# Kernel tuning notes

Measured on AMD Instinct MI355X. Metric: run time of the kernel, lower is better.

The kernel has to match this reference:

```python
import jax, jax.numpy as jnp
import numpy as np

B, C, H, W = 16, 256, 32, 32  # C == emb_dim
NUM_EMB = 8192


def setup_inputs() -> dict:
    key = jax.random.key(0)
    k1, k2 = jax.random.split(key)
    z_e = jax.random.normal(k1, (B, C, H, W), dtype=jnp.float32)
    # torch init: uniform(-1/num_emb, 1/num_emb); randn spec scaled to similar magnitude
    embedding = jax.random.uniform(k2, (NUM_EMB, C), dtype=jnp.float32,
                                   minval=-1.0 / NUM_EMB, maxval=1.0 / NUM_EMB)
    return {"z_e": z_e, "embedding": embedding}


def reference(z_e, embedding):
    num_emb, emb_dim = embedding.shape
    # [B, C, H, W] -> [B, H, W, C]
    z = jnp.transpose(z_e, (0, 2, 3, 1))
    flat = z.reshape(-1, emb_dim)  # [N, C]
    # squared L2 distances via ||z||^2 + ||e||^2 - 2 z.e  (the addmm)
    emb_sqr = jnp.sum(embedding * embedding, axis=1)            # [K]
    z_sqr = jnp.sum(flat * flat, axis=1, keepdims=True)         # [N, 1]
    distances = z_sqr + emb_sqr[None, :] - 2.0 * (flat @ embedding.T)  # [N, K]
    indices = jnp.argmin(distances, axis=1)                     # [N]
    z_q = embedding[indices].reshape(z.shape)                   # gather -> [B,H,W,C]
    z_one_hot = jax.nn.one_hot(indices, num_emb, dtype=jnp.float32)  # [N, K]
    # straight-through estimator
    z_q = z + jax.lax.stop_gradient(z_q - z)
    return (z, z_q, indices, z_one_hot)
```

## Files before the change

kernel.cpp:

```cpp
#include <hip/hip_runtime.h>
#include <stdint.h>

typedef unsigned long long u64;
typedef unsigned u32;
typedef __attribute__((ext_vector_type(8))) _Float16 half8;
typedef __attribute__((ext_vector_type(4))) float f32x4;

#define NROWS 16384
#define CDIM  256
#define NEMB  8192

#define Z_OFF   0ull
#define ZQ_OFF  4194304ull
#define IDX_OFF 8388608ull
#define OH_OFF  8404992ull

#define ES_OFF_BYTES     0
#define ZS_OFF_BYTES     32768
#define ORIENT_OFF_BYTES 98304
#define KEYSA_OFF_BYTES  131072
#define KEYSB_OFF_BYTES  4325376
#define EHL_ROW0 16128

#define ESCALE 512.0f
#define INV2SCALE 0.00390625f

#define THR_ULP 4u
#define TRIP_ULP 8u

__device__ __forceinline__ u32 fmap(float x) {
    u32 u = __float_as_uint(x);
    return (u & 0x80000000u) ? ~u : (u | 0x80000000u);
}
__device__ __forceinline__ u32 udiff(u32 a, u32 b) { return a > b ? a - b : b - a; }

__device__ __forceinline__ void gload_lds16(const char* g, char* l) {
    __builtin_amdgcn_global_load_lds(
        (const __attribute__((address_space(1))) void*)(g),
        (__attribute__((address_space(3))) void*)(l), 16, 0, 0);
}

__global__ __launch_bounds__(256) void k_transpose(const float* __restrict__ ze,
                                                   float* __restrict__ z) {
    __shared__ float T[64][65];
    int b = blockIdx.z, ct = blockIdx.x, ht = blockIdx.y;
    int c0 = ct * 64, hw0 = ht * 64;
    int lane = threadIdx.x & 63, grp = threadIdx.x >> 6;
    #pragma unroll
    for (int i = 0; i < 16; ++i) {
        int cl = grp + i * 4;
        T[cl][lane] = ze[((size_t)(b * 256 + c0 + cl)) * 1024 + hw0 + lane];
    }
    __syncthreads();
    #pragma unroll
    for (int i = 0; i < 16; ++i) {
        int hwl = grp + i * 4;
        z[((size_t)(b * 1024 + hw0 + hwl)) * 256 + c0 + lane] = T[lane][hwl];
    }
}

__device__ __forceinline__ float pw128sq(const float* __restrict__ x) {
    float r[8];
    #pragma unroll
    for (int j = 0; j < 8; ++j) r[j] = __fmul_rn(x[j], x[j]);
    #pragma unroll
    for (int i = 8; i < 128; i += 8) {
        #pragma unroll
        for (int j = 0; j < 8; ++j)
            r[j] = __fadd_rn(r[j], __fmul_rn(x[i + j], x[i + j]));
    }
    return __fadd_rn(__fadd_rn(__fadd_rn(r[0], r[1]), __fadd_rn(r[2], r[3])),
                     __fadd_rn(__fadd_rn(r[4], r[5]), __fadd_rn(r[6], r[7])));
}

__global__ __launch_bounds__(256) void k_rowsq(const float* __restrict__ X,
                                               float* __restrict__ out,
                                               int nrows) {
    int r = blockIdx.x * 256 + threadIdx.x;
    if (r >= nrows) return;
    const float* x = &X[(size_t)r * 256];
    out[r] = __fadd_rn(pw128sq(x), pw128sq(x + 128));
}

__global__ __launch_bounds__(256) void k_zsq(const float* __restrict__ ze,
                                             float* __restrict__ zs) {
    int t = blockIdx.x * 256 + threadIdx.x;
    int b = t >> 10, hw = t & 1023;
    const float* base = ze + ((size_t)b * 256) * 1024 + hw;
    float half[2];
    #pragma unroll
    for (int hB = 0; hB < 2; ++hB) {
        const float* p = base + (size_t)(hB * 128) * 1024;
        float r[8];
        #pragma unroll
        for (int j = 0; j < 8; ++j) {
            float v = p[(size_t)j * 1024];
            r[j] = __fmul_rn(v, v);
        }
        #pragma unroll
        for (int i = 8; i < 128; i += 8) {
            #pragma unroll
            for (int j = 0; j < 8; ++j) {
                float v = p[(size_t)(i + j) * 1024];
                r[j] = __fadd_rn(r[j], __fmul_rn(v, v));
            }
        }
        half[hB] = __fadd_rn(__fadd_rn(__fadd_rn(r[0], r[1]), __fadd_rn(r[2], r[3])),
                             __fadd_rn(__fadd_rn(r[4], r[5]), __fadd_rn(r[6], r[7])));
    }
    zs[t] = __fadd_rn(half[0], half[1]);
}

__global__ __launch_bounds__(256) void k_split16(const float* __restrict__ X,
                                                 char* __restrict__ H,
                                                 int nrows, float scale) {
    int t = blockIdx.x * 256 + threadIdx.x;
    if (t >= nrows * 32) return;
    int row = t >> 5, c8 = t & 31;
    const float* src = X + (size_t)row * 256 + c8 * 8;
    float4 f0 = *(const float4*)src;
    float4 f1 = *(const float4*)(src + 4);
    float f[8] = {f0.x, f0.y, f0.z, f0.w, f1.x, f1.y, f1.z, f1.w};
    union { _Float16 h[8]; uint4 v; } u;
    #pragma unroll
    for (int j = 0; j < 8; ++j)
        u.h[j] = (_Float16)(f[j] * scale);
    int rb = row >> 7, rloc = row & 127, kc = c8 >> 2, p = c8 & 3;
    size_t base = ((size_t)(rb * 8 + kc)) * 8192 + (size_t)p * 2048 + (size_t)rloc * 16;
    *(uint4*)(H + base) = u.v;
}

__global__ __launch_bounds__(256) void k_dist(const char* __restrict__ ZH,
                                              const char* __restrict__ EH,
                                              const float* __restrict__ es,
                                              const float* __restrict__ zs,
                                              u32* __restrict__ keysA,
                                              u32* __restrict__ keysB) {
    __shared__ __align__(16) char smem[21504];
    int bx = blockIdx.x;
    int by = blockIdx.y;
    int tid = threadIdx.x;
    int w = tid >> 6, lane = tid & 63;
    int p = lane >> 4, l15 = lane & 15;
    int rowhalf = (w & 1) * 64, colhalf = (w >> 1) * 64;
    int row0 = by * 128, col0 = bx * 128;

    f32x4 acc[4][4] = {};

    const char* asrc = ZH + ((size_t)(by * 8)) * 8192;
    const char* bsrc = EH + ((size_t)(bx * 8)) * 8192;

    for (int kc = 0; kc < 8; ++kc) {
        if (kc) __syncthreads();
        const char* ak = asrc + (size_t)kc * 8192;
        const char* bk = bsrc + (size_t)kc * 8192;
        #pragma unroll
        for (int it = 0; it < 2; ++it) {
            int off = it * 4096 + tid * 16;
            gload_lds16(ak + off, smem + off);
        }
        #pragma unroll
        for (int it = 0; it < 2; ++it) {
            int off = it * 4096 + tid * 16;
            gload_lds16(bk + off, smem + 8192 + off);
        }
        __syncthreads();

        half8 A[4], B[4];
        #pragma unroll
        for (int rt = 0; rt < 4; ++rt) {
            int r = rowhalf + rt * 16 + l15;
            A[rt] = *(const half8*)(smem + p * 2048 + r * 16);
        }
        #pragma unroll
        for (int ct = 0; ct < 4; ++ct) {
            int c = colhalf + ct * 16 + l15;
            B[ct] = *(const half8*)(smem + 8192 + p * 2048 + c * 16);
        }
        #pragma unroll
        for (int rt = 0; rt < 4; ++rt)
            #pragma unroll
            for (int ct = 0; ct < 4; ++ct)
                acc[rt][ct] = __builtin_amdgcn_mfma_f32_16x16x32_f16(
                    A[rt], B[ct], acc[rt][ct], 0, 0, 0);
    }
    __syncthreads();

    u32* redA = (u32*)smem;
    u32* redB = (u32*)(smem + 16896);

    float esA[4], zsB4[4], esB[4][4], zsA[4][4];
    #pragma unroll
    for (int ct = 0; ct < 4; ++ct) {
        esA[ct] = es[col0 + colhalf + ct * 16 + l15];
        #pragma unroll
        for (int reg = 0; reg < 4; ++reg)
            esB[ct][reg] = es[col0 + colhalf + ct * 16 + p * 4 + reg];
    }
    #pragma unroll
    for (int rt = 0; rt < 4; ++rt) {
        zsB4[rt] = zs[row0 + rowhalf + rt * 16 + l15];
        #pragma unroll
        for (int reg = 0; reg < 4; ++reg)
            zsA[rt][reg] = zs[row0 + rowhalf + rt * 16 + p * 4 + reg];
    }

    #pragma unroll
    for (int rt = 0; rt < 4; ++rt) {
        u32 bB = 0xffffffffu;
        #pragma unroll
        for (int reg = 0; reg < 4; ++reg) {
            u32 bA = 0xffffffffu;
            #pragma unroll
            for (int ct = 0; ct < 4; ++ct) {
                float a2 = __fmul_rn(acc[rt][ct][reg], INV2SCALE);
                float vA = __fsub_rn(__fadd_rn(zsA[rt][reg], esA[ct]), a2);
                float vB = __fsub_rn(__fadd_rn(zsB4[rt], esB[ct][reg]), a2);
                u32 fA = fmap(vA), fB = fmap(vB);
                if (fA < bA) bA = fA;
                if (fB < bB) bB = fB;
            }
            redA[(rowhalf + rt * 16 + p * 4 + reg) * 33 + (w >> 1) * 16 + l15] = bA;
        }
        redB[(rowhalf + rt * 16 + l15) * 9 + (w >> 1) * 4 + p] = bB;
    }
    __syncthreads();
    if (tid < 128) {
        u32 bA = 0xffffffffu, bB = 0xffffffffu;
        #pragma unroll
        for (int s = 0; s < 32; ++s) { u32 v = redA[tid * 33 + s]; if (v < bA) bA = v; }
        #pragma unroll
        for (int s = 0; s < 8; ++s)  { u32 v = redB[tid * 9 + s];  if (v < bB) bB = v; }
        keysA[((size_t)(row0 + tid)) * 64 + bx] = bA;
        keysB[((size_t)(row0 + tid)) * 64 + bx] = bB;
    }
}

__device__ __forceinline__ u64 exact_key4(const float* zrow, const float* __restrict__ E,
                                          const float* __restrict__ es, float zsn, int k) {
    const float4* e4 = (const float4*)&E[(size_t)k * 256];
    float dot = 0.0f;
    #pragma unroll 4
    for (int c4 = 0; c4 < 64; ++c4) {
        float4 ev = e4[c4];
        dot = fmaf(zrow[c4 * 4 + 0], ev.x, dot);
        dot = fmaf(zrow[c4 * 4 + 1], ev.y, dot);
        dot = fmaf(zrow[c4 * 4 + 2], ev.z, dot);
        dot = fmaf(zrow[c4 * 4 + 3], ev.w, dot);
    }
    float t1 = __fadd_rn(zsn, es[k]);
    float d  = __fsub_rn(t1, __fmul_rn(2.0f, dot));
    return ((u64)fmap(d) << 32) | (u32)k;
}

__global__ __launch_bounds__(256) void k_orient(const float* __restrict__ Z,
                                                const float* __restrict__ E,
                                                const float* __restrict__ es,
                                                const float* __restrict__ zs,
                                                const u32* __restrict__ keysA,
                                                const u32* __restrict__ keysB,
                                                int* __restrict__ orient) {
    __shared__ float zrow[256];
    __shared__ u32 mex[256];
    int tid = threadIdx.x;
    zrow[tid] = Z[tid];
    __syncthreads();
    int chunk = tid >> 4, sub = tid & 15;
    float zsn = zs[0];
    u32 best = 0xffffffffu;
    #pragma unroll 2
    for (int j = 0; j < 8; ++j) {
        u64 key = exact_key4(zrow, E, es, zsn, chunk * 128 + sub * 8 + j);
        u32 f = (u32)(key >> 32);
        if (f < best) best = f;
    }
    mex[tid] = best;
    __syncthreads();
    if (tid == 0) {
        int cA = 0, cB = 0;
        for (int s = 0; s < 16; ++s) {
            u32 m = 0xffffffffu;
            for (int t = 0; t < 16; ++t) { u32 v = mex[s * 16 + t]; if (v < m) m = v; }
            if (udiff(keysA[s], m) <= 2u) ++cA;
            if (udiff(keysB[s], m) <= 2u) ++cB;
        }
        *orient = (cA >= 12) ? 0 : (cB >= 12) ? 1 : 2;
    }
}

__global__ __launch_bounds__(256) void k_final(const float* __restrict__ Z,
                                               const float* __restrict__ E,
                                               const float* __restrict__ es,
                                               const float* __restrict__ zs,
                                               const u32* __restrict__ keysA,
                                               const u32* __restrict__ keysB,
                                               const int* __restrict__ orient,
                                               float* __restrict__ zq,
                                               float* __restrict__ idxf,
                                               float* __restrict__ oh) {
    __shared__ float zrow[256];
    __shared__ u32 kch[64];
    __shared__ u64 rmin[256];
    __shared__ int flaglist[64];
    __shared__ int nflag;
    __shared__ u32 mval;
    __shared__ int strip;

    int n = blockIdx.x, tid = threadIdx.x;
    int ori = *orient;
    const u32* keys = (ori == 1) ? keysB : keysA;

    zrow[tid] = Z[(size_t)n * 256 + tid];
    if (tid < 64) kch[tid] = keys[(size_t)n * 64 + tid];
    __syncthreads();
    if (tid == 0) {
        if (ori == 2) {
            nflag = 64;
            for (int s = 0; s < 64; ++s) flaglist[s] = s;
            mval = 0;
        } else {
            u32 m = 0xffffffffu;
            for (int s = 0; s < 64; ++s) if (kch[s] < m) m = kch[s];
            u32 thr = m + THR_ULP;
            int nf = 0;
            for (int s = 0; s < 64; ++s) if (kch[s] <= thr) flaglist[nf++] = s;
            nflag = nf; mval = m;
        }
    }
    __syncthreads();

    float zsn = zs[n];
    u64 best = ~0ull;
    {
        int tot = nflag * 128;
        for (int i = tid; i < tot; i += 256) {
            u64 key = exact_key4(zrow, E, es, zsn,
                                 flaglist[i >> 7] * 128 + (i & 127));
            if (key < best) best = key;
        }
    }
    rmin[tid] = best;
    __syncthreads();
    for (int s = 128; s > 0; s >>= 1) {
        if (tid < s) { if (rmin[tid + s] < rmin[tid]) rmin[tid] = rmin[tid + s]; }
        __syncthreads();
    }
    u64 ph1 = rmin[0];
    if (tid == 0)
        strip = (ori != 2) && (udiff((u32)(ph1 >> 32), mval) > TRIP_ULP);
    __syncthreads();

    if (strip) {
        best = ~0ull;
        for (int i = tid; i < NEMB; i += 256) {
            u64 key = exact_key4(zrow, E, es, zsn, i);
            if (key < best) best = key;
        }
        rmin[tid] = best;
        __syncthreads();
        for (int s = 128; s > 0; s >>= 1) {
            if (tid < s) { if (rmin[tid + s] < rmin[tid]) rmin[tid] = rmin[tid + s]; }
            __syncthreads();
        }
    }
    int idx = (int)(rmin[0] & 0xffffffffu);

    if (n >= EHL_ROW0) {
        float* ohrow = oh + (size_t)n * NEMB;
        float4 z4 = make_float4(0.f, 0.f, 0.f, 0.f);
        #pragma unroll
        for (int it = 0; it < 8; ++it)
            *(float4*)&ohrow[(it * 256 + tid) * 4] = z4;
        __syncthreads();
    }

    if (tid < 64)
        *(float4*)&zq[(size_t)n * 256 + tid * 4] =
            *(const float4*)&E[(size_t)idx * 256 + tid * 4];
    if (tid == 0) {
        idxf[n] = (float)idx;
        oh[(size_t)n * NEMB + idx] = 1.0f;
    }
}

extern "C" void kernel_launch(void* const* d_in, const int* in_sizes, int n_in,
                              void* d_out, int out_size, void* d_ws, size_t ws_size,
                              hipStream_t stream) {
    const float* ze  = (const float*)d_in[0];
    const float* emb = (const float*)d_in[1];
    float* out = (float*)d_out;
    float* z    = out + Z_OFF;
    float* zq   = out + ZQ_OFF;
    float* idxf = out + IDX_OFF;
    float* oh   = out + OH_OFF;
    float* es    = (float*)((char*)d_ws + ES_OFF_BYTES);
    float* zs    = (float*)((char*)d_ws + ZS_OFF_BYTES);
    int*   orient= (int*)((char*)d_ws + ORIENT_OFF_BYTES);
    u32*   keysA = (u32*)((char*)d_ws + KEYSA_OFF_BYTES);
    u32*   keysB = (u32*)((char*)d_ws + KEYSB_OFF_BYTES);
    char*  ZH   = (char*)zq;
    char*  EH   = (char*)(oh + (size_t)EHL_ROW0 * NEMB);

    k_transpose<<<dim3(4, 16, 16), 256, 0, stream>>>(ze, z);
    k_zsq<<<NROWS / 256, 256, 0, stream>>>(ze, zs);
    k_rowsq<<<NEMB / 256, 256, 0, stream>>>(emb, es, NEMB);
    k_split16<<<NROWS * 32 / 256, 256, 0, stream>>>(z, ZH, NROWS, 1.0f);
    k_split16<<<NEMB * 32 / 256, 256, 0, stream>>>(emb, EH, NEMB, ESCALE);
    k_dist<<<dim3(64, 128), 256, 0, stream>>>(ZH, EH, es, zs, keysA, keysB);
    k_orient<<<1, 256, 0, stream>>>(z, emb, es, zs, keysA, keysB, orient);
    k_final<<<NROWS, 256, 0, stream>>>(z, emb, es, zs, keysA, keysB, orient,
                                       zq, idxf, oh);
}
```

Before: 978.4 us.

## Refine candidate selection to 32-column groups using packed per-group key deltas

The distance kernel now reduces each 128-column tile in two halves, giving four 32-column group minima per row. It packs their offsets from the tile minimum into 4-bit fields for both orientations and writes them to a scratch buffer placed in the one-hot output tail. The final kernel uses these deltas to rescan only the 32-column groups whose approximate key is within threshold, rather than whole 128-column tiles, cutting exact fp32 rescoring work. The cost is an extra barrier and reduction pass in the distance epilogue, and a new tail kernel to zero and fill the one-hot rows that held the scratch buffer.

```diff
diff --git a/kernel.cpp b/kernel.cpp
--- a/kernel.cpp
+++ b/kernel.cpp
@@ -21,6 +21,7 @@
 #define KEYSA_OFF_BYTES  131072
 #define KEYSB_OFF_BYTES  4325376
 #define EHL_ROW0 16128
+#define DROW0    16256
 
 #define ESCALE 512.0f
 #define INV2SCALE 0.00390625f
@@ -135,7 +136,8 @@
                                               const float* __restrict__ es,
                                               const float* __restrict__ zs,
                                               u32* __restrict__ keysA,
-                                              u32* __restrict__ keysB) {
+                                              u32* __restrict__ keysB,
+                                              u32* __restrict__ dAB) {
     __shared__ __align__(16) char smem[21504];
     int bx = blockIdx.x;
     int by = blockIdx.y;
@@ -205,34 +207,69 @@
             zsA[rt][reg] = zs[row0 + rowhalf + rt * 16 + p * 4 + reg];
     }
 
-    #pragma unroll
-    for (int rt = 0; rt < 4; ++rt) {
-        u32 bB = 0xffffffffu;
-        #pragma unroll
-        for (int reg = 0; reg < 4; ++reg) {
-            u32 bA = 0xffffffffu;
+    u32 gA[4], gB[4];
+    #pragma unroll
+    for (int half = 0; half < 2; ++half) {
+        if (half) __syncthreads();
+        #pragma unroll
+        for (int rt = 0; rt < 4; ++rt) {
+            u32 bB = 0xffffffffu;
             #pragma unroll
-            for (int ct = 0; ct < 4; ++ct) {
-                float a2 = __fmul_rn(acc[rt][ct][reg], INV2SCALE);
-                float vA = __fsub_rn(__fadd_rn(zsA[rt][reg], esA[ct]), a2);
-                float vB = __fsub_rn(__fadd_rn(zsB4[rt], esB[ct][reg]), a2);
-                u32 fA = fmap(vA), fB = fmap(vB);
-                if (fA < bA) bA = fA;
-                if (fB < bB) bB = fB;
+            for (int reg = 0; reg < 4; ++reg) {
+                u32 bA = 0xffffffffu;
+                #pragma unroll
+                for (int c2 = 0; c2 < 2; ++c2) {
+                    int ct = half * 2 + c2;
+                    float a2 = __fmul_rn(acc[rt][ct][reg], INV2SCALE);
+                    float vA = __fsub_rn(__fadd_rn(zsA[rt][reg], esA[ct]), a2);
+                    float vB = __fsub_rn(__fadd_rn(zsB4[rt], esB[ct][reg]), a2);
+                    u32 fA = fmap(vA), fB = fmap(vB);
+                    if (fA < bA) bA = fA;
+                    if (fB < bB) bB = fB;
+                }
+                redA[(rowhalf + rt * 16 + p * 4 + reg) * 33 + (w >> 1) * 16 + l15] = bA;
             }
-            redA[(rowhalf + rt * 16 + p * 4 + reg) * 33 + (w >> 1) * 16 + l15] = bA;
-        }
-        redB[(rowhalf + rt * 16 + l15) * 9 + (w >> 1) * 4 + p] = bB;
-    }
-    __syncthreads();
+            redB[(rowhalf + rt * 16 + l15) * 9 + (w >> 1) * 4 + p] = bB;
+        }
+        __syncthreads();
+        if (tid < 128) {
+            #pragma unroll
+            for (int h = 0; h < 2; ++h) {
+                u32 mA = 0xffffffffu;
+                #pragma unroll
+                for (int s = 0; s < 16; ++s) {
+                    u32 v = redA[tid * 33 + h * 16 + s];
+                    if (v < mA) mA = v;
+                }
+                gA[h * 2 + half] = mA;
+                u32 mB = 0xffffffffu;
+                #pragma unroll
+                for (int s = 0; s < 4; ++s) {
+                    u32 v = redB[tid * 9 + h * 4 + s];
+                    if (v < mB) mB = v;
+                }
+                gB[h * 2 + half] = mB;
+            }
+        }
+    }
+
     if (tid < 128) {
-        u32 bA = 0xffffffffu, bB = 0xffffffffu;
-        #pragma unroll
-        for (int s = 0; s < 32; ++s) { u32 v = redA[tid * 33 + s]; if (v < bA) bA = v; }
-        #pragma unroll
-        for (int s = 0; s < 8; ++s)  { u32 v = redB[tid * 9 + s];  if (v < bB) bB = v; }
+        u32 bA = gA[0], bB = gB[0];
+        #pragma unroll
+        for (int g = 1; g < 4; ++g) {
+            if (gA[g] < bA) bA = gA[g];
+            if (gB[g] < bB) bB = gB[g];
+        }
         keysA[((size_t)(row0 + tid)) * 64 + bx] = bA;
         keysB[((size_t)(row0 + tid)) * 64 + bx] = bB;
+        u32 dword = 0;
+        #pragma unroll
+        for (int g = 0; g < 4; ++g) {
+            u32 dA = gA[g] - bA; if (dA > 15u) dA = 15u;
+            u32 dB = gB[g] - bB; if (dB > 15u) dB = 15u;
+            dword |= (dA << (4 * g)) | (dB << (16 + 4 * g));
+        }
+        dAB[((size_t)(row0 + tid)) * 64 + bx] = dword;
     }
 }
 
@@ -294,15 +331,17 @@
                                                const float* __restrict__ zs,
                                                const u32* __restrict__ keysA,
                                                const u32* __restrict__ keysB,
+                                               const u32* __restrict__ dAB,
                                                const int* __restrict__ orient,
                                                float* __restrict__ zq,
                                                float* __restrict__ idxf,
                                                float* __restrict__ oh) {
     __shared__ float zrow[256];
     __shared__ u32 kch[64];
+    __shared__ u32 dv[64];
     __shared__ u64 rmin[256];
-    __shared__ int flaglist[64];
-    __shared__ int nflag;
+    __shared__ short glist[256];
+    __shared__ int ng;
     __shared__ u32 mval;
     __shared__ int strip;
 
@@ -311,20 +350,32 @@
     const u32* keys = (ori == 1) ? keysB : keysA;
 
     zrow[tid] = Z[(size_t)n * 256 + tid];
-    if (tid < 64) kch[tid] = keys[(size_t)n * 64 + tid];
+    if (tid < 64) {
+        kch[tid] = keys[(size_t)n * 64 + tid];
+        dv[tid]  = dAB[(size_t)n * 64 + tid];
+    }
     __syncthreads();
     if (tid == 0) {
         if (ori == 2) {
-            nflag = 64;
-            for (int s = 0; s < 64; ++s) flaglist[s] = s;
+            ng = 256;
+            for (int i = 0; i < 256; ++i) glist[i] = (short)i;
             mval = 0;
         } else {
             u32 m = 0xffffffffu;
             for (int s = 0; s < 64; ++s) if (kch[s] < m) m = kch[s];
             u32 thr = m + THR_ULP;
-            int nf = 0;
-            for (int s = 0; s < 64; ++s) if (kch[s] <= thr) flaglist[nf++] = s;
-            nflag = nf; mval = m;
+            int cnt = 0;
+            for (int s = 0; s < 64; ++s) {
+                u32 base = kch[s];
+                if (base > thr) continue;
+                u32 sel = (ori == 1) ? (dv[s] >> 16) : (dv[s] & 0xffffu);
+                #pragma unroll
+                for (int g = 0; g < 4; ++g) {
+                    u32 d = (sel >> (4 * g)) & 0xfu;
+                    if (base + d <= thr) glist[cnt++] = (short)(s * 4 + g);
+                }
+            }
+            ng = cnt; mval = m;
         }
     }
     __syncthreads();
@@ -332,10 +383,11 @@
     float zsn = zs[n];
     u64 best = ~0ull;
     {
-        int tot = nflag * 128;
+        int tot = ng * 32;
         for (int i = tid; i < tot; i += 256) {
+            int v = glist[i >> 5];
             u64 key = exact_key4(zrow, E, es, zsn,
-                                 flaglist[i >> 7] * 128 + (i & 127));
+                                 (v >> 2) * 128 + (v & 3) * 32 + (i & 31));
             if (key < best) best = key;
         }
     }
@@ -365,7 +417,7 @@
     }
     int idx = (int)(rmin[0] & 0xffffffffu);
 
-    if (n >= EHL_ROW0) {
+    if (n >= EHL_ROW0 && n < DROW0) {
         float* ohrow = oh + (size_t)n * NEMB;
         float4 z4 = make_float4(0.f, 0.f, 0.f, 0.f);
         #pragma unroll
@@ -379,8 +431,22 @@
             *(const float4*)&E[(size_t)idx * 256 + tid * 4];
     if (tid == 0) {
         idxf[n] = (float)idx;
-        oh[(size_t)n * NEMB + idx] = 1.0f;
-    }
+        if (n < DROW0) oh[(size_t)n * NEMB + idx] = 1.0f;
+    }
+}
+
+__global__ __launch_bounds__(256) void k_ohtail(const float* __restrict__ idxf,
+                                                float* __restrict__ oh) {
+    int n = DROW0 + blockIdx.x;
+    int tid = threadIdx.x;
+    float* ohrow = oh + (size_t)n * NEMB;
+    float4 z4 = make_float4(0.f, 0.f, 0.f, 0.f);
+    #pragma unroll
+    for (int it = 0; it < 8; ++it)
+        *(float4*)&ohrow[(it * 256 + tid) * 4] = z4;
+    __syncthreads();
+    if (tid == 0)
+        ohrow[(int)idxf[n]] = 1.0f;
 }
 
 extern "C" void kernel_launch(void* const* d_in, const int* in_sizes, int n_in,
@@ -400,14 +466,16 @@
     u32*   keysB = (u32*)((char*)d_ws + KEYSB_OFF_BYTES);
     char*  ZH   = (char*)zq;
     char*  EH   = (char*)(oh + (size_t)EHL_ROW0 * NEMB);
+    u32*   dAB  = (u32*)(EH + 4 * 1024 * 1024);
 
     k_transpose<<<dim3(4, 16, 16), 256, 0, stream>>>(ze, z);
     k_zsq<<<NROWS / 256, 256, 0, stream>>>(ze, zs);
     k_rowsq<<<NEMB / 256, 256, 0, stream>>>(emb, es, NEMB);
     k_split16<<<NROWS * 32 / 256, 256, 0, stream>>>(z, ZH, NROWS, 1.0f);
     k_split16<<<NEMB * 32 / 256, 256, 0, stream>>>(emb, EH, NEMB, ESCALE);
-    k_dist<<<dim3(64, 128), 256, 0, stream>>>(ZH, EH, es, zs, keysA, keysB);
+    k_dist<<<dim3(64, 128), 256, 0, stream>>>(ZH, EH, es, zs, keysA, keysB, dAB);
     k_orient<<<1, 256, 0, stream>>>(z, emb, es, zs, keysA, keysB, orient);
-    k_final<<<NROWS, 256, 0, stream>>>(z, emb, es, zs, keysA, keysB, orient,
+    k_final<<<NROWS, 256, 0, stream>>>(z, emb, es, zs, keysA, keysB, dAB, orient,
                                        zq, idxf, oh);
-}
+    k_ohtail<<<NROWS - DROW0, 256, 0, stream>>>(idxf, oh);
+}
```

Result: faster. 832.8 us (-14.9%).
